# Kernel optimization log

Hardware: AMD Instinct MI355X
Metric: run time of the kernel (lower is better)

## Reference

```python
import jax, jax.numpy as jnp
import numpy as np

B, T, S, E, H, F = 4, 1024, 1024, 512, 8, 2048
D = E // H  # head_dim = 64
SCALE = D ** -0.5
EPS = 1e-5


def setup_inputs() -> dict:
    key = jax.random.key(0)
    ks = jax.random.split(key, 16)
    w = lambda k, shape: jax.random.normal(k, shape, jnp.float32) * 0.02
    inp = {
        'tgt': jax.random.normal(ks[0], (B, T, E), jnp.float32),
        'memory': jax.random.normal(ks[1], (B, S, E), jnp.float32),
    }
    for i, n in enumerate(['sWq', 'sWk', 'sWv', 'sWo', 'cWq', 'cWk', 'cWv', 'cWo']):
        inp[n] = w(ks[2 + i], (E, E))
    for n in ['sbq', 'sbk', 'sbv', 'sbo', 'cbq', 'cbk', 'cbv', 'cbo']:
        inp[n] = jnp.zeros((E,), jnp.float32)
    inp['fW1'] = w(ks[10], (E, F)); inp['fb1'] = jnp.zeros((F,), jnp.float32)
    inp['fW2'] = w(ks[11], (F, E)); inp['fb2'] = jnp.zeros((E,), jnp.float32)
    for n in ['g1', 'g2', 'g3']:
        inp[n] = jnp.ones((E,), jnp.float32)
    for n in ['be1', 'be2', 'be3']:
        inp[n] = jnp.zeros((E,), jnp.float32)
    return inp


def _ln(x, g, b):
    mu = jnp.mean(x, axis=-1, keepdims=True)
    var = jnp.mean(jnp.square(x - mu), axis=-1, keepdims=True)
    return (x - mu) * jax.lax.rsqrt(var + EPS) * g + b


def _mha(xq, xkv, Wq, bq, Wk, bk, Wv, bv, Wo, bo):
    # dense-equivalent of full N^2 edge-list attention (softmax over source nodes per target)
    Bq, Tq, _ = xq.shape
    Skv = xkv.shape[1]
    q = (xq @ Wq + bq).reshape(Bq, Tq, H, D)
    k = (xkv @ Wk + bk).reshape(Bq, Skv, H, D)
    v = (xkv @ Wv + bv).reshape(Bq, Skv, H, D)
    scores = jnp.einsum('bthd,bshd->bhts', q, k) * SCALE
    wts = jax.nn.softmax(scores, axis=-1)
    out = jnp.einsum('bhts,bshd->bthd', wts, v).reshape(Bq, Tq, E)
    return out @ Wo + bo


def reference(tgt, memory,
              sWq, sbq, sWk, sbk, sWv, sbv, sWo, sbo,
              cWq, cbq, cWk, cbk, cWv, cbv, cWo, cbo,
              fW1, fb1, fW2, fb2,
              g1, be1, g2, be2, g3, be3):
    # post-norm decoder layer: self-attn -> cross-attn -> FFN (dropout=0 eval)
    x = _ln(tgt + _mha(tgt, tgt, sWq, sbq, sWk, sbk, sWv, sbv, sWo, sbo), g1, be1)
    x = _ln(x + _mha(x, memory, cWq, cbq, cWk, cbk, cWv, cbv, cWo, cbo), g2, be2)
    ff = jax.nn.relu(x @ fW1 + fb1) @ fW2 + fb2
    x = _ln(x + ff, g3, be3)
    return x
```

## Files before the change

kernel.cpp:

```cpp
#include <hip/hip_runtime.h>

typedef unsigned short ushort_t;
typedef short short8 __attribute__((ext_vector_type(8)));
typedef float float4v __attribute__((ext_vector_type(4)));

__device__ __forceinline__ float bf2f(ushort_t u) {
    union { unsigned int i; float f; } x; x.i = ((unsigned int)u) << 16; return x.f;
}
__device__ __forceinline__ ushort_t f2bf(float f) {
    unsigned int u = __float_as_uint(f);
    unsigned int r = (u + 0x7FFFu + ((u >> 16) & 1u)) >> 16;
    return (ushort_t)r;
}
__device__ __forceinline__ void store_out(float* p, float v) { *p = v; }
__device__ __forceinline__ void store_out(ushort_t* p, float v) { *p = f2bf(v); }

__device__ __forceinline__ void gll16(const ushort_t* g, ushort_t* l) {
    __builtin_amdgcn_global_load_lds(
        (const __attribute__((address_space(1))) void*)g,
        (__attribute__((address_space(3))) void*)l, 16, 0, 0);
}

__global__ void detect_dtype(const ushort_t* __restrict__ tgt, int* __restrict__ flag) {
    __shared__ int red[256];
    const int tid = threadIdx.x;
    int p = 0;
    for (int i = tid; i < 512; i += 256) {
        ushort_t u = tgt[i];
        int e = (u >> 7) & 0xFF;
        if (u == 0 || (e >= 100 && e <= 140)) ++p;
    }
    red[tid] = p; __syncthreads();
    for (int off = 128; off > 0; off >>= 1) {
        if (tid < off) red[tid] += red[tid + off];
        __syncthreads();
    }
    if (tid == 0) flag[0] = (red[0] >= 480) ? 1 : 0;
}

__device__ __forceinline__ bool is_f32(int mode, const int* dflag) {
    return (mode == 2) ? (dflag[0] == 0) : (mode == 0);
}

__global__ __launch_bounds__(256) void prep_all(
    const void* sWq, const void* sWk, const void* sWv, const void* sWo,
    const void* cWq, const void* cWk, const void* cWv, const void* cWo,
    const void* fW1, const void* fW2,
    const void* tgt, const void* mem,
    const void* sbq, const void* sbk, const void* sbv, const void* sbo,
    const void* cbq, const void* cbk, const void* cbv, const void* cbo,
    const void* fb1, const void* fb2,
    ushort_t* __restrict__ wb, ushort_t* __restrict__ tb, ushort_t* __restrict__ mb,
    float* __restrict__ pb, int mode, const int* __restrict__ dflag)
{
    const bool f32 = is_f32(mode, dflag);
    const int tid = threadIdx.x;
    const int id = blockIdx.x;

    if (id < 1024) {
        int z, kt, nt;
        if (id < 512)      { z = id >> 6;  int t = id & 63;  kt = t >> 3; nt = t & 7;  }
        else if (id < 768) { z = 8;        int t = id - 512; kt = t >> 5; nt = t & 31; }
        else               { z = 9;        int t = id - 768; kt = t >> 3; nt = t & 7;  }
        const void* src; ushort_t* dst; int Kd, Nd;
        switch (z) {
            case 0: src = sWq; dst = wb + 0;       Kd = 512;  Nd = 512;  break;
            case 1: src = sWk; dst = wb + 262144;  Kd = 512;  Nd = 512;  break;
            case 2: src = sWv; dst = wb + 524288;  Kd = 512;  Nd = 512;  break;
            case 3: src = sWo; dst = wb + 786432;  Kd = 512;  Nd = 512;  break;
            case 4: src = cWq; dst = wb + 1048576; Kd = 512;  Nd = 512;  break;
            case 5: src = cWk; dst = wb + 1310720; Kd = 512;  Nd = 512;  break;
            case 6: src = cWv; dst = wb + 1572864; Kd = 512;  Nd = 512;  break;
            case 7: src = cWo; dst = wb + 1835008; Kd = 512;  Nd = 512;  break;
            case 8: src = fW1; dst = wb + 2097152; Kd = 512;  Nd = 2048; break;
            default:src = fW2; dst = wb + 3145728; Kd = 2048; Nd = 512;  break;
        }
        const int k0 = kt * 64, n0 = nt * 64;
        __shared__ ushort_t T[64][65];
#pragma unroll
        for (int i = 0; i < 16; ++i) {
            int j = i * 256 + tid;
            int r = j >> 6, c = j & 63;
            float v = f32 ? ((const float*)src)[(size_t)(k0 + r) * Nd + n0 + c]
                          : bf2f(((const ushort_t*)src)[(size_t)(k0 + r) * Nd + n0 + c]);
            T[r][c] = f2bf(v);
        }
        __syncthreads();
#pragma unroll
        for (int i = 0; i < 16; ++i) {
            int j = i * 256 + tid;
            int n = j >> 6, k = j & 63;
            dst[(size_t)(n0 + n) * Kd + k0 + k] = T[k][n];
        }
        return;
    }

    if (id < 3072) {
        const int bid0 = id - 1024;
        const void* src = (bid0 < 1024) ? tgt : mem;
        ushort_t* dst = (bid0 < 1024) ? tb : mb;
        const int bid = bid0 & 1023;
        const int i = (bid * 256 + tid) * 8;
        if (f32) {
            float4 v0 = *(const float4*)((const float*)src + i);
            float4 v1 = *(const float4*)((const float*)src + i + 4);
            ushort_t o[8] = { f2bf(v0.x), f2bf(v0.y), f2bf(v0.z), f2bf(v0.w),
                              f2bf(v1.x), f2bf(v1.y), f2bf(v1.z), f2bf(v1.w) };
            *(uint4*)(dst + i) = *(const uint4*)o;
        } else {
            *(uint4*)(dst + i) = *(const uint4*)((const ushort_t*)src + i);
        }
        return;
    }

    {
        const int i = (id - 3072) * 256 + tid;
        if (i >= 6656) return;
        const void* src; int off;
        if      (i < 512)  { src = sbq; off = i; }
        else if (i < 1024) { src = sbk; off = i - 512; }
        else if (i < 1536) { src = sbv; off = i - 1024; }
        else if (i < 2048) { src = sbo; off = i - 1536; }
        else if (i < 2560) { src = cbq; off = i - 2048; }
        else if (i < 3072) { src = cbk; off = i - 2560; }
        else if (i < 3584) { src = cbv; off = i - 3072; }
        else if (i < 4096) { src = cbo; off = i - 3584; }
        else if (i < 6144) { src = fb1; off = i - 4096; }
        else               { src = fb2; off = i - 6144; }
        pb[i] = f32 ? ((const float*)src)[off] : bf2f(((const ushort_t*)src)[off]);
    }
}

template<typename OutT, bool RELU, int BM, int BN, bool KSPLIT>
__global__ __launch_bounds__(256, (BM == 64) ? 3 : 2) void gemm_tn(
    const ushort_t* __restrict__ A1, const ushort_t* __restrict__ A2,
    int ySplit, int lda,
    const ushort_t* __restrict__ Wt, int ldw,
    const float* __restrict__ bias,
    OutT* __restrict__ C, int ldc, int K,
    OutT* __restrict__ C2)
{
    constexpr int WC = (BM == 64 && BN == 128) ? 4 : 2;
    constexpr int WR = 4 / WC;
    constexpr int MI = BM / (WR * 16);
    constexpr int NI = BN / (WC * 16);
    __shared__ ushort_t As[2][2][BM][32];
    __shared__ ushort_t Bs[2][2][BN][32];
    const int tid = threadIdx.x;
    const int wave = tid >> 6, lane = tid & 63;
    const int quad = lane >> 4, l16 = lane & 15;
    const int m0 = blockIdx.x * BM, n0 = blockIdx.y * BN;
    const int wm = (wave / WC) * (BM / WR);
    const int wn = (wave % WC) * (BN / WC);
    const ushort_t* A = (((int)blockIdx.y) < ySplit) ? A1 : A2;
    const ushort_t* W = Wt;
    OutT* Cw = C;
    bool second = false;
    if (KSPLIT && blockIdx.z) { A += K; W += K; Cw = C2; second = true; }

    float4v acc[MI][NI];
#pragma unroll
    for (int mi = 0; mi < MI; ++mi)
#pragma unroll
        for (int ni = 0; ni < NI; ++ni) {
            acc[mi][ni][0] = 0.f; acc[mi][ni][1] = 0.f;
            acc[mi][ni][2] = 0.f; acc[mi][ni][3] = 0.f;
        }

    const int srow = lane >> 2;
    const int scc  = lane & 3;
    const int sg   = (scc - (lane >> 3)) & 3;
    const ushort_t* aptr0 = A  + (size_t)(m0 + wave * 16 + srow) * lda + sg * 8;
    const ushort_t* aptr1 = A  + (size_t)(m0 + 64 + wave * 16 + srow) * lda + sg * 8;
    const ushort_t* bptr0 = W + (size_t)(n0 + wave * 16 + srow) * ldw + sg * 8;
    const ushort_t* bptr1 = W + (size_t)(n0 + 64 + wave * 16 + srow) * ldw + sg * 8;

    gll16(aptr0,      &As[0][0][wave * 16][0]);
    gll16(aptr0 + 32, &As[0][1][wave * 16][0]);
    if (BM == 128) {
        gll16(aptr1,      &As[0][0][64 + wave * 16][0]);
        gll16(aptr1 + 32, &As[0][1][64 + wave * 16][0]);
    }
    gll16(bptr0,      &Bs[0][0][wave * 16][0]);
    gll16(bptr0 + 32, &Bs[0][1][wave * 16][0]);
    if (BN == 128) {
        gll16(bptr1,      &Bs[0][0][64 + wave * 16][0]);
        gll16(bptr1 + 32, &Bs[0][1][64 + wave * 16][0]);
    }

    const int ca = ((quad + (l16 >> 1)) & 3) * 8;
    int cur = 0;
    for (int k0 = 0; k0 < K; k0 += 64) {
        __syncthreads();
        if (k0 + 64 < K) {
            const int nb = cur ^ 1, ko = k0 + 64;
            gll16(aptr0 + ko,      &As[nb][0][wave * 16][0]);
            gll16(aptr0 + ko + 32, &As[nb][1][wave * 16][0]);
            if (BM == 128) {
                gll16(aptr1 + ko,      &As[nb][0][64 + wave * 16][0]);
                gll16(aptr1 + ko + 32, &As[nb][1][64 + wave * 16][0]);
            }
            gll16(bptr0 + ko,      &Bs[nb][0][wave * 16][0]);
            gll16(bptr0 + ko + 32, &Bs[nb][1][wave * 16][0]);
            if (BN == 128) {
                gll16(bptr1 + ko,      &Bs[nb][0][64 + wave * 16][0]);
                gll16(bptr1 + ko + 32, &Bs[nb][1][64 + wave * 16][0]);
            }
        }
#pragma unroll
        for (int kk = 0; kk < 2; ++kk) {
            short8 af[MI], bfr[NI];
#pragma unroll
            for (int mi = 0; mi < MI; ++mi)
                af[mi] = *(const short8*)(&As[cur][kk][wm + mi * 16 + l16][ca]);
#pragma unroll
            for (int ni = 0; ni < NI; ++ni)
                bfr[ni] = *(const short8*)(&Bs[cur][kk][wn + ni * 16 + l16][ca]);
#pragma unroll
            for (int mi = 0; mi < MI; ++mi)
#pragma unroll
                for (int ni = 0; ni < NI; ++ni)
                    acc[mi][ni] = __builtin_amdgcn_mfma_f32_16x16x32_bf16(
                        af[mi], bfr[ni], acc[mi][ni], 0, 0, 0);
        }
        cur ^= 1;
    }

#pragma unroll
    for (int ni = 0; ni < NI; ++ni) {
        const int col = n0 + wn + ni * 16 + l16;
        const float bv = (KSPLIT && second) ? 0.f : bias[col];
#pragma unroll
        for (int mi = 0; mi < MI; ++mi)
#pragma unroll
            for (int r = 0; r < 4; ++r) {
                const int row = m0 + wm + mi * 16 + quad * 4 + r;
                float v = acc[mi][ni][r] + bv;
                if (RELU) v = fmaxf(v, 0.f);
                store_out(&Cw[(size_t)row * ldc + col], v);
            }
    }
}

__global__ __launch_bounds__(512) void attn_mfma(ushort_t* __restrict__ QKV)
{
    const int S = 1536;
    __shared__ ushort_t PsA[64][72];
    __shared__ ushort_t PsB[64][72];
    __shared__ ushort_t Ks[2][64][72];
    __shared__ ushort_t Vt[2][64][72];

    const int tid  = threadIdx.x;
    const int w    = tid >> 6;
    const int g    = w >> 2;
    const int wq   = w & 3;
    const int lane = tid & 63;
    const int quad = lane >> 4, l16 = lane & 15;
    const int ht   = tid & 255;
    const int qt = blockIdx.x, bh = blockIdx.y;
    const int b = bh >> 3, h = bh & 7;
    const size_t rowQ = (size_t)b * 1024 + qt * 64;
    const size_t kv0  = (size_t)b * 1024;

    const int kr = ht >> 2, kc = (ht & 3) * 16;
    const int sp = ht >> 3, dc = (ht & 7) * 8;
    const int vr0 = sp * 2;
    const int vrg = vr0 >> 3, vrof = vr0 & 7;

    {
        const int r = tid >> 3, c = (tid & 7) * 8;
        *(uint4*)(&PsA[r][c]) = *(const uint4*)(QKV + (rowQ + r) * S + h * 64 + c);
    }
    __syncthreads();
    short8 qf[2];
    qf[0] = *(const short8*)(&PsA[wq * 16 + l16][quad * 8]);
    qf[1] = *(const short8*)(&PsA[wq * 16 + l16][32 + quad * 8]);
    ushort_t (* __restrict__ Ps)[72] = g ? PsB : PsA;

    const float CEXP = 0.125f * 1.44269504f;
    const float MREF = 16.0f * CEXP;
    float lsum[4];
    float4v oacc[4];
#pragma unroll
    for (int r = 0; r < 4; ++r) lsum[r] = 0.f;
#pragma unroll
    for (int n = 0; n < 4; ++n) { oacc[n][0]=0.f; oacc[n][1]=0.f; oacc[n][2]=0.f; oacc[n][3]=0.f; }

    uint4 kA, kB, vA, vB;
    {
        const size_t sr = kv0 + g * 64;
        const ushort_t* ksrc = QKV + (sr + kr) * S + 512 + h * 64 + kc;
        kA = *(const uint4*)(ksrc);
        kB = *(const uint4*)(ksrc + 8);
        const ushort_t* vsrc = QKV + (sr + vr0) * S + 1024 + h * 64 + dc;
        vA = *(const uint4*)(vsrc);
        vB = *(const uint4*)(vsrc + S);
    }

    for (int it = 0; it < 8; ++it) {
        __syncthreads();
        *(uint4*)(&Ks[g][kr][kc])     = kA;
        *(uint4*)(&Ks[g][kr][kc + 8]) = kB;
        {
            const ushort_t* ae = (const ushort_t*)&vA;
            const ushort_t* be = (const ushort_t*)&vB;
#pragma unroll
            for (int j = 0; j < 8; ++j) {
                const int d = dc + j;
                const int cc = (vrg ^ (d >> 4)) & 7;
                *(unsigned int*)(&Vt[g][d][cc * 8 + vrof]) =
                    (unsigned int)ae[j] | ((unsigned int)be[j] << 16);
            }
        }
        __syncthreads();
        if (it < 7) {
            const size_t sr = kv0 + (it + 1) * 128 + g * 64;
            const ushort_t* ksrc = QKV + (sr + kr) * S + 512 + h * 64 + kc;
            kA = *(const uint4*)(ksrc);
            kB = *(const uint4*)(ksrc + 8);
            const ushort_t* vsrc = QKV + (sr + vr0) * S + 1024 + h * 64 + dc;
            vA = *(const uint4*)(vsrc);
            vB = *(const uint4*)(vsrc + S);
        }

        float4v sc[4];
#pragma unroll
        for (int sb = 0; sb < 4; ++sb) {
            float4v z; z[0]=0.f; z[1]=0.f; z[2]=0.f; z[3]=0.f;
            short8 kf0 = *(const short8*)(&Ks[g][sb * 16 + l16][quad * 8]);
            short8 kf1 = *(const short8*)(&Ks[g][sb * 16 + l16][32 + quad * 8]);
            z = __builtin_amdgcn_mfma_f32_16x16x32_bf16(qf[0], kf0, z, 0, 0, 0);
            z = __builtin_amdgcn_mfma_f32_16x16x32_bf16(qf[1], kf1, z, 0, 0, 0);
            sc[sb] = z;
        }

#pragma unroll
        for (int sb = 0; sb < 4; ++sb)
#pragma unroll
            for (int r = 0; r < 4; ++r) {
                float p = exp2f(fmaf(sc[sb][r], CEXP, -MREF));
                lsum[r] += p;
                Ps[wq * 16 + quad * 4 + r][sb * 16 + l16] = f2bf(p);
            }

        short8 pf[2];
        pf[0] = *(const short8*)(&Ps[wq * 16 + l16][quad * 8]);
        pf[1] = *(const short8*)(&Ps[wq * 16 + l16][32 + quad * 8]);
#pragma unroll
        for (int n = 0; n < 4; ++n) {
#pragma unroll
            for (int kc2 = 0; kc2 < 2; ++kc2) {
                const int cc = ((kc2 * 4 + quad) ^ n) & 7;
                short8 vf = *(const short8*)(&Vt[g][n * 16 + l16][cc * 8]);
                oacc[n] = __builtin_amdgcn_mfma_f32_16x16x32_bf16(pf[kc2], vf, oacc[n], 0, 0, 0);
            }
        }
    }

#pragma unroll
    for (int msk = 1; msk < 16; msk <<= 1)
#pragma unroll
        for (int r = 0; r < 4; ++r) lsum[r] += __shfl_xor(lsum[r], msk);

    float* exch = (float*)&Ks[0][0][0];
    float* exl  = (float*)&Vt[0][0][0];
    __syncthreads();
    if (g == 1) {
#pragma unroll
        for (int n = 0; n < 4; ++n)
#pragma unroll
            for (int r = 0; r < 4; ++r)
                exch[((wq * 4 + n) * 4 + r) * 64 + lane] = oacc[n][r];
        if (l16 == 0)
#pragma unroll
            for (int r = 0; r < 4; ++r) exl[wq * 16 + quad * 4 + r] = lsum[r];
    }
    __syncthreads();
    if (g == 0) {
#pragma unroll
        for (int r = 0; r < 4; ++r) lsum[r] += exl[wq * 16 + quad * 4 + r];
        float inv[4];
#pragma unroll
        for (int r = 0; r < 4; ++r) inv[r] = 1.f / lsum[r];
#pragma unroll
        for (int n = 0; n < 4; ++n)
#pragma unroll
            for (int r = 0; r < 4; ++r) {
                float o = oacc[n][r] + exch[((wq * 4 + n) * 4 + r) * 64 + lane];
                const size_t row = rowQ + wq * 16 + quad * 4 + r;
                QKV[row * S + h * 64 + n * 16 + l16] = f2bf(o * inv[r]);
            }
    }
}

template<bool RES_EXT, bool OUT_EXT>
__global__ __launch_bounds__(256) void ln_kernel(
    const void* __restrict__ res,
    const ushort_t* __restrict__ d1, const ushort_t* __restrict__ d2,
    const void* __restrict__ g, const void* __restrict__ be,
    void* __restrict__ out, int mode, const int* __restrict__ dflag)
{
    const int E = 512;
    const bool extf32 = is_f32(mode, dflag);
    const int row = blockIdx.x, tid = threadIdx.x;
    const int wave = tid >> 6, lane = tid & 63;
    const size_t base = (size_t)row * E;
    const int i0 = tid, i1 = tid + 256;

    float r0, r1;
    if (RES_EXT && extf32) {
        r0 = ((const float*)res)[base + i0];
        r1 = ((const float*)res)[base + i1];
    } else {
        r0 = bf2f(((const ushort_t*)res)[base + i0]);
        r1 = bf2f(((const ushort_t*)res)[base + i1]);
    }
    float d0v = bf2f(d1[base + i0]) + bf2f(d2[base + i0]);
    float d1v = bf2f(d1[base + i1]) + bf2f(d2[base + i1]);
    float x0 = r0 + d0v, x1 = r1 + d1v;

    __shared__ float red8[8];
    float s = x0 + x1;
#pragma unroll
    for (int m = 1; m < 64; m <<= 1) s += __shfl_xor(s, m);
    if (lane == 0) red8[wave] = s;
    __syncthreads();
    float mean = (red8[0] + red8[1] + red8[2] + red8[3]) * (1.0f / 512.0f);
    float dd0 = x0 - mean, dd1 = x1 - mean;
    float v = dd0 * dd0 + dd1 * dd1;
#pragma unroll
    for (int m = 1; m < 64; m <<= 1) v += __shfl_xor(v, m);
    if (lane == 0) red8[4 + wave] = v;
    __syncthreads();
    float rstd = rsqrtf((red8[4] + red8[5] + red8[6] + red8[7]) * (1.0f / 512.0f) + 1e-5f);

    float g0, g1v, b0, b1;
    if (extf32) {
        g0 = ((const float*)g)[i0];  g1v = ((const float*)g)[i1];
        b0 = ((const float*)be)[i0]; b1  = ((const float*)be)[i1];
    } else {
        g0 = bf2f(((const ushort_t*)g)[i0]);  g1v = bf2f(((const ushort_t*)g)[i1]);
        b0 = bf2f(((const ushort_t*)be)[i0]); b1  = bf2f(((const ushort_t*)be)[i1]);
    }
    float y0 = dd0 * rstd * g0 + b0;
    float y1 = dd1 * rstd * g1v + b1;
    if (OUT_EXT && extf32) {
        ((float*)out)[base + i0] = y0; ((float*)out)[base + i1] = y1;
    } else {
        ((ushort_t*)out)[base + i0] = f2bf(y0);
        ((ushort_t*)out)[base + i1] = f2bf(y1);
    }
}


extern "C" void kernel_launch(void* const* d_in, const int* in_sizes, int n_in,
                              void* d_out, int out_size, void* d_ws, size_t ws_size,
                              hipStream_t stream) {
    const void* tgt = d_in[0];
    const void* mem = d_in[1];
    const void* sWq = d_in[2];  const void* sWk = d_in[3];
    const void* sWv = d_in[4];  const void* sWo = d_in[5];
    const void* cWq = d_in[6];  const void* cWk = d_in[7];
    const void* cWv = d_in[8];  const void* cWo = d_in[9];
    const void* sbq = d_in[10]; const void* sbk = d_in[11];
    const void* sbv = d_in[12]; const void* sbo = d_in[13];
    const void* cbq = d_in[14]; const void* cbk = d_in[15];
    const void* cbv = d_in[16]; const void* cbo = d_in[17];
    const void* fW1 = d_in[18]; const void* fb1 = d_in[19];
    const void* fW2 = d_in[20]; const void* fb2 = d_in[21];
    const void* g1  = d_in[22]; const void* g2  = d_in[23];
    const void* g3  = d_in[24];
    const void* be1 = d_in[25]; const void* be2 = d_in[26];
    const void* be3 = d_in[27];

    char* ws = (char*)d_ws;
    const size_t MB = 1048576;
    ushort_t* qkv = (ushort_t*)(ws + 0 * MB);
    ushort_t* hb  = (ushort_t*)(ws + 0 * MB);
    ushort_t* pA  = (ushort_t*)(ws + 12 * MB);
    ushort_t* xb  = (ushort_t*)(ws + 16 * MB);
    ushort_t* tb  = (ushort_t*)(ws + 20 * MB);
    ushort_t* mb  = (ushort_t*)(ws + 24 * MB);
    ushort_t* pB  = (ushort_t*)(ws + 20 * MB);
    ushort_t* ofA = (ushort_t*)(ws + 20 * MB);
    ushort_t* ofB = (ushort_t*)(ws + 24 * MB);
    ushort_t* wb  = (ushort_t*)(ws + 28 * MB);
    float*    pb  = (float*)   (ws + 36 * MB);
    int*   dflag  = (int*)     (ws + 36 * MB + 262144);

    const ushort_t* sWqkv_t = wb + 0;
    const ushort_t* sWo_t   = wb + 786432;
    const ushort_t* cWqkv_t = wb + 1048576;
    const ushort_t* cWo_t   = wb + 1835008;
    const ushort_t* fW1_t   = wb + 2097152;
    const ushort_t* fW2_t   = wb + 3145728;

    dim3 blk(256);

    int mode;
    if (in_sizes[0] == 4 * 1024 * 512 * 4)      mode = 0;
    else if (in_sizes[0] == 4 * 1024 * 512 * 2) mode = 1;
    else                                        mode = 2;
    if (mode == 2)
        detect_dtype<<<dim3(1), blk, 0, stream>>>((const ushort_t*)tgt, dflag);

    prep_all<<<dim3(3098), blk, 0, stream>>>(
        sWq, sWk, sWv, sWo, cWq, cWk, cWv, cWo, fW1, fW2,
        tgt, mem, sbq, sbk, sbv, sbo, cbq, cbk, cbv, cbo, fb1, fb2,
        wb, tb, mb, pb, mode, dflag);

    dim3 gattn(16, 32);
    dim3 blk512(512);

    gemm_tn<ushort_t, false, 64, 128, false><<<dim3(64, 12), blk, 0, stream>>>(
        tb, tb, 0, 512, sWqkv_t, 512, pb + 0, qkv, 1536, 512, (ushort_t*)nullptr);
    attn_mfma<<<gattn, blk512, 0, stream>>>(qkv);
    gemm_tn<ushort_t, false, 64, 64, true><<<dim3(64, 8, 2), blk, 0, stream>>>(
        qkv, qkv, 0, 1536, sWo_t, 512, pb + 1536, pA, 512, 256, pB);
    ln_kernel<true, false><<<dim3(4096), blk, 0, stream>>>(
        tgt, pA, pB, g1, be1, xb, mode, dflag);

    gemm_tn<ushort_t, false, 64, 128, false><<<dim3(64, 12), blk, 0, stream>>>(
        xb, mb, 4, 512, cWqkv_t, 512, pb + 2048, qkv, 1536, 512, (ushort_t*)nullptr);
    attn_mfma<<<gattn, blk512, 0, stream>>>(qkv);
    gemm_tn<ushort_t, false, 64, 64, true><<<dim3(64, 8, 2), blk, 0, stream>>>(
        qkv, qkv, 0, 1536, cWo_t, 512, pb + 3584, pA, 512, 256, pB);
    ln_kernel<false, false><<<dim3(4096), blk, 0, stream>>>(
        xb, pA, pB, g2, be2, xb, mode, dflag);

    gemm_tn<ushort_t, true, 128, 128, false><<<dim3(32, 16), blk, 0, stream>>>(
        xb, xb, 0, 512, fW1_t, 512, pb + 4096, hb, 2048, 512, (ushort_t*)nullptr);
    gemm_tn<ushort_t, false, 64, 64, true><<<dim3(64, 8, 2), blk, 0, stream>>>(
        hb, hb, 0, 2048, fW2_t, 2048, pb + 6144, ofA, 512, 1024, ofB);
    ln_kernel<false, true><<<dim3(4096), blk, 0, stream>>>(
        xb, ofA, ofB, g3, be3, d_out, mode, dflag);
}
```

Measured before the change: 266.5 us.

## Shrink FFN GEMM tiles, add BN=32 variant, vectorize LayerNorm loads

Changes the FFN up-projection GEMM from 128x128 to 64x128 tiles and the down-projection from 64x64 to 64x32 tiles, adding a BN=32 path in which only two waves stage B and occupancy is raised to 4. The aim is more blocks to fill the GPU's compute units for these GEMMs. The LayerNorm kernel now gives each thread two adjacent elements, loaded and stored as paired 32-bit or float2 accesses. Smaller tiles cut data reuse and raise global traffic per FLOP, and the BN=32 path depends on the warp layout code handling NI correctly.

```diff
diff --git a/kernel.cpp b/kernel.cpp
--- a/kernel.cpp
+++ b/kernel.cpp
@@ -132,7 +132,8 @@
 }
 
 template<typename OutT, bool RELU, int BM, int BN, bool KSPLIT>
-__global__ __launch_bounds__(256, (BM == 64) ? 3 : 2) void gemm_tn(
+__global__ __launch_bounds__(256, (BM == 64 && BN == 32) ? 4 : ((BM == 64) ? 3 : 2))
+void gemm_tn(
     const ushort_t* __restrict__ A1, const ushort_t* __restrict__ A2,
     int ySplit, int lda,
     const ushort_t* __restrict__ Wt, int ldw,
@@ -158,6 +159,8 @@
     bool second = false;
     if (KSPLIT && blockIdx.z) { A += K; W += K; Cw = C2; second = true; }
 
+    const bool bstage = (BN >= 64) || (wave < 2);
+
     float4v acc[MI][NI];
 #pragma unroll
     for (int mi = 0; mi < MI; ++mi)
@@ -181,8 +184,10 @@
         gll16(aptr1,      &As[0][0][64 + wave * 16][0]);
         gll16(aptr1 + 32, &As[0][1][64 + wave * 16][0]);
     }
-    gll16(bptr0,      &Bs[0][0][wave * 16][0]);
-    gll16(bptr0 + 32, &Bs[0][1][wave * 16][0]);
+    if (bstage) {
+        gll16(bptr0,      &Bs[0][0][wave * 16][0]);
+        gll16(bptr0 + 32, &Bs[0][1][wave * 16][0]);
+    }
     if (BN == 128) {
         gll16(bptr1,      &Bs[0][0][64 + wave * 16][0]);
         gll16(bptr1 + 32, &Bs[0][1][64 + wave * 16][0]);
@@ -200,8 +205,10 @@
                 gll16(aptr1 + ko,      &As[nb][0][64 + wave * 16][0]);
                 gll16(aptr1 + ko + 32, &As[nb][1][64 + wave * 16][0]);
             }
-            gll16(bptr0 + ko,      &Bs[nb][0][wave * 16][0]);
-            gll16(bptr0 + ko + 32, &Bs[nb][1][wave * 16][0]);
+            if (bstage) {
+                gll16(bptr0 + ko,      &Bs[nb][0][wave * 16][0]);
+                gll16(bptr0 + ko + 32, &Bs[nb][1][wave * 16][0]);
+            }
             if (BN == 128) {
                 gll16(bptr1 + ko,      &Bs[nb][0][64 + wave * 16][0]);
                 gll16(bptr1 + ko + 32, &Bs[nb][1][64 + wave * 16][0]);
@@ -405,18 +412,20 @@
     const int row = blockIdx.x, tid = threadIdx.x;
     const int wave = tid >> 6, lane = tid & 63;
     const size_t base = (size_t)row * E;
-    const int i0 = tid, i1 = tid + 256;
+    const int i0 = tid * 2;
 
     float r0, r1;
     if (RES_EXT && extf32) {
-        r0 = ((const float*)res)[base + i0];
-        r1 = ((const float*)res)[base + i1];
+        float2 rv = *(const float2*)((const float*)res + base + i0);
+        r0 = rv.x; r1 = rv.y;
     } else {
-        r0 = bf2f(((const ushort_t*)res)[base + i0]);
-        r1 = bf2f(((const ushort_t*)res)[base + i1]);
-    }
-    float d0v = bf2f(d1[base + i0]) + bf2f(d2[base + i0]);
-    float d1v = bf2f(d1[base + i1]) + bf2f(d2[base + i1]);
+        unsigned int rv = *(const unsigned int*)((const ushort_t*)res + base + i0);
+        r0 = bf2f((ushort_t)rv); r1 = bf2f((ushort_t)(rv >> 16));
+    }
+    unsigned int u1 = *(const unsigned int*)(d1 + base + i0);
+    unsigned int u2 = *(const unsigned int*)(d2 + base + i0);
+    float d0v = bf2f((ushort_t)u1) + bf2f((ushort_t)u2);
+    float d1v = bf2f((ushort_t)(u1 >> 16)) + bf2f((ushort_t)(u2 >> 16));
     float x0 = r0 + d0v, x1 = r1 + d1v;
 
     __shared__ float red8[8];
@@ -436,19 +445,23 @@
 
     float g0, g1v, b0, b1;
     if (extf32) {
-        g0 = ((const float*)g)[i0];  g1v = ((const float*)g)[i1];
-        b0 = ((const float*)be)[i0]; b1  = ((const float*)be)[i1];
+        float2 gv = *(const float2*)((const float*)g + i0);
+        float2 bv = *(const float2*)((const float*)be + i0);
+        g0 = gv.x; g1v = gv.y; b0 = bv.x; b1 = bv.y;
     } else {
-        g0 = bf2f(((const ushort_t*)g)[i0]);  g1v = bf2f(((const ushort_t*)g)[i1]);
-        b0 = bf2f(((const ushort_t*)be)[i0]); b1  = bf2f(((const ushort_t*)be)[i1]);
+        unsigned int gv = *(const unsigned int*)((const ushort_t*)g + i0);
+        unsigned int bv = *(const unsigned int*)((const ushort_t*)be + i0);
+        g0 = bf2f((ushort_t)gv);  g1v = bf2f((ushort_t)(gv >> 16));
+        b0 = bf2f((ushort_t)bv);  b1  = bf2f((ushort_t)(bv >> 16));
     }
     float y0 = dd0 * rstd * g0 + b0;
     float y1 = dd1 * rstd * g1v + b1;
     if (OUT_EXT && extf32) {
-        ((float*)out)[base + i0] = y0; ((float*)out)[base + i1] = y1;
+        float2 ov; ov.x = y0; ov.y = y1;
+        *(float2*)((float*)out + base + i0) = ov;
     } else {
-        ((ushort_t*)out)[base + i0] = f2bf(y0);
-        ((ushort_t*)out)[base + i1] = f2bf(y1);
+        unsigned int ov = (unsigned int)f2bf(y0) | ((unsigned int)f2bf(y1) << 16);
+        *(unsigned int*)((ushort_t*)out + base + i0) = ov;
     }
 }
 
@@ -528,9 +541,9 @@
     ln_kernel<false, false><<<dim3(4096), blk, 0, stream>>>(
         xb, pA, pB, g2, be2, xb, mode, dflag);
 
-    gemm_tn<ushort_t, true, 128, 128, false><<<dim3(32, 16), blk, 0, stream>>>(
+    gemm_tn<ushort_t, true, 64, 128, false><<<dim3(64, 16), blk, 0, stream>>>(
         xb, xb, 0, 512, fW1_t, 512, pb + 4096, hb, 2048, 512, (ushort_t*)nullptr);
-    gemm_tn<ushort_t, false, 64, 64, true><<<dim3(64, 8, 2), blk, 0, stream>>>(
+    gemm_tn<ushort_t, false, 64, 32, true><<<dim3(64, 16, 2), blk, 0, stream>>>(
         hb, hb, 0, 2048, fW2_t, 2048, pb + 6144, ofA, 512, 1024, ofB);
     ln_kernel<false, true><<<dim3(4096), blk, 0, stream>>>(
         xb, ofA, ofB, g3, be3, d_out, mode, dflag);
```

Result: slower. 276.7 us (+3.9%).

## Merge self-attn output projection with cross-attn K/V projection in one launch

Applied to the files above, without the earlier changes.

Adds a combined kernel that runs the self-attention output-projection GEMM blocks and the memory-side K/V projection GEMM blocks of cross-attention together in a single grid, sharing a common LDS pool. The K/V projection depends only on `memory`, so it is hoisted ahead of LayerNorm 1 to fill the GPU alongside the small split-K output projection. The later cross-attention projection launch now computes only the Q columns. This removes one launch and raises occupancy of an under-filled GEMM. The cost is mixed tile shapes in one grid, which can cause load imbalance, and correctness relies on the two halves touching disjoint column ranges of the qkv buffer.

```diff
diff --git a/kernel.cpp b/kernel.cpp
--- a/kernel.cpp
+++ b/kernel.cpp
@@ -128,6 +128,145 @@
         else if (i < 6144) { src = fb1; off = i - 4096; }
         else               { src = fb2; off = i - 6144; }
         pb[i] = f32 ? ((const float*)src)[off] : bf2f(((const ushort_t*)src)[off]);
+    }
+}
+
+template<typename OutT, bool RELU, int BM, int BN, bool KSPLIT>
+__device__ __forceinline__ void gemm_body(ushort_t* pool, int bx, int by, int bz,
+    const ushort_t* __restrict__ A1, const ushort_t* __restrict__ A2,
+    int ySplit, int lda,
+    const ushort_t* __restrict__ Wt, int ldw,
+    const float* __restrict__ bias,
+    OutT* __restrict__ C, int ldc, int K,
+    OutT* __restrict__ C2)
+{
+    constexpr int WC = (BM == 64 && BN == 128) ? 4 : 2;
+    constexpr int WR = 4 / WC;
+    constexpr int MI = BM / (WR * 16);
+    constexpr int NI = BN / (WC * 16);
+    ushort_t* Asp = pool;
+    ushort_t* Bsp = pool + 128 * BM;
+
+    const int tid = threadIdx.x;
+    const int wave = tid >> 6, lane = tid & 63;
+    const int quad = lane >> 4, l16 = lane & 15;
+    const int m0 = bx * BM, n0 = by * BN;
+    const int wm = (wave / WC) * (BM / WR);
+    const int wn = (wave % WC) * (BN / WC);
+    const ushort_t* A = (by < ySplit) ? A1 : A2;
+    const ushort_t* W = Wt;
+    OutT* Cw = C;
+    bool second = false;
+    if (KSPLIT && bz) { A += K; W += K; Cw = C2; second = true; }
+
+    float4v acc[MI][NI];
+#pragma unroll
+    for (int mi = 0; mi < MI; ++mi)
+#pragma unroll
+        for (int ni = 0; ni < NI; ++ni) {
+            acc[mi][ni][0] = 0.f; acc[mi][ni][1] = 0.f;
+            acc[mi][ni][2] = 0.f; acc[mi][ni][3] = 0.f;
+        }
+
+    const int srow = lane >> 2;
+    const int scc  = lane & 3;
+    const int sg   = (scc - (lane >> 3)) & 3;
+    const ushort_t* aptr0 = A + (size_t)(m0 + wave * 16 + srow) * lda + sg * 8;
+    const ushort_t* aptr1 = A + (size_t)(m0 + 64 + wave * 16 + srow) * lda + sg * 8;
+    const ushort_t* bptr0 = W + (size_t)(n0 + wave * 16 + srow) * ldw + sg * 8;
+    const ushort_t* bptr1 = W + (size_t)(n0 + 64 + wave * 16 + srow) * ldw + sg * 8;
+
+    auto As = [&](int buf, int kk, int row) -> ushort_t* {
+        return Asp + (size_t)((buf * 2 + kk) * BM + row) * 32;
+    };
+    auto Bs = [&](int buf, int kk, int row) -> ushort_t* {
+        return Bsp + (size_t)((buf * 2 + kk) * BN + row) * 32;
+    };
+
+    gll16(aptr0,      As(0, 0, wave * 16));
+    gll16(aptr0 + 32, As(0, 1, wave * 16));
+    if (BM == 128) {
+        gll16(aptr1,      As(0, 0, 64 + wave * 16));
+        gll16(aptr1 + 32, As(0, 1, 64 + wave * 16));
+    }
+    gll16(bptr0,      Bs(0, 0, wave * 16));
+    gll16(bptr0 + 32, Bs(0, 1, wave * 16));
+    if (BN == 128) {
+        gll16(bptr1,      Bs(0, 0, 64 + wave * 16));
+        gll16(bptr1 + 32, Bs(0, 1, 64 + wave * 16));
+    }
+
+    const int ca = ((quad + (l16 >> 1)) & 3) * 8;
+    int cur = 0;
+    for (int k0 = 0; k0 < K; k0 += 64) {
+        __syncthreads();
+        if (k0 + 64 < K) {
+            const int nb = cur ^ 1, ko = k0 + 64;
+            gll16(aptr0 + ko,      As(nb, 0, wave * 16));
+            gll16(aptr0 + ko + 32, As(nb, 1, wave * 16));
+            if (BM == 128) {
+                gll16(aptr1 + ko,      As(nb, 0, 64 + wave * 16));
+                gll16(aptr1 + ko + 32, As(nb, 1, 64 + wave * 16));
+            }
+            gll16(bptr0 + ko,      Bs(nb, 0, wave * 16));
+            gll16(bptr0 + ko + 32, Bs(nb, 1, wave * 16));
+            if (BN == 128) {
+                gll16(bptr1 + ko,      Bs(nb, 0, 64 + wave * 16));
+                gll16(bptr1 + ko + 32, Bs(nb, 1, 64 + wave * 16));
+            }
+        }
+#pragma unroll
+        for (int kk = 0; kk < 2; ++kk) {
+            short8 af[MI], bfr[NI];
+#pragma unroll
+            for (int mi = 0; mi < MI; ++mi)
+                af[mi] = *(const short8*)(As(cur, kk, wm + mi * 16 + l16) + ca);
+#pragma unroll
+            for (int ni = 0; ni < NI; ++ni)
+                bfr[ni] = *(const short8*)(Bs(cur, kk, wn + ni * 16 + l16) + ca);
+#pragma unroll
+            for (int mi = 0; mi < MI; ++mi)
+#pragma unroll
+                for (int ni = 0; ni < NI; ++ni)
+                    acc[mi][ni] = __builtin_amdgcn_mfma_f32_16x16x32_bf16(
+                        af[mi], bfr[ni], acc[mi][ni], 0, 0, 0);
+        }
+        cur ^= 1;
+    }
+
+#pragma unroll
+    for (int ni = 0; ni < NI; ++ni) {
+        const int col = n0 + wn + ni * 16 + l16;
+        const float bv = (KSPLIT && second) ? 0.f : bias[col];
+#pragma unroll
+        for (int mi = 0; mi < MI; ++mi)
+#pragma unroll
+            for (int r = 0; r < 4; ++r) {
+                const int row = m0 + wm + mi * 16 + quad * 4 + r;
+                float v = acc[mi][ni][r] + bv;
+                if (RELU) v = fmaxf(v, 0.f);
+                store_out(&Cw[(size_t)row * ldc + col], v);
+            }
+    }
+}
+
+__global__ __launch_bounds__(256, 3) void oproj_ckv(
+    const ushort_t* __restrict__ qkv_in, const ushort_t* __restrict__ sWo_t,
+    const float* __restrict__ bias_o,
+    ushort_t* __restrict__ pA, ushort_t* __restrict__ pB,
+    const ushort_t* __restrict__ mb, const ushort_t* __restrict__ cWqkv_t,
+    const float* __restrict__ bias_c, ushort_t* __restrict__ qkv_out)
+{
+    __shared__ ushort_t pool[24576];
+    const int t = blockIdx.x;
+    if (t < 1024) {
+        gemm_body<ushort_t, false, 64, 64, true>(pool, t & 63, (t >> 6) & 7, t >> 9,
+            qkv_in, qkv_in, 0, 1536, sWo_t, 512, bias_o, pA, 512, 256, pB);
+    } else {
+        const int t2 = t - 1024;
+        gemm_body<ushort_t, false, 64, 128, false>(pool, t2 & 63, 4 + (t2 >> 6), 0,
+            mb, mb, 4, 512, cWqkv_t, 512, bias_c, qkv_out, 1536, 512,
+            (ushort_t*)nullptr);
     }
 }
 
@@ -515,12 +654,12 @@
     gemm_tn<ushort_t, false, 64, 128, false><<<dim3(64, 12), blk, 0, stream>>>(
         tb, tb, 0, 512, sWqkv_t, 512, pb + 0, qkv, 1536, 512, (ushort_t*)nullptr);
     attn_mfma<<<gattn, blk512, 0, stream>>>(qkv);
-    gemm_tn<ushort_t, false, 64, 64, true><<<dim3(64, 8, 2), blk, 0, stream>>>(
-        qkv, qkv, 0, 1536, sWo_t, 512, pb + 1536, pA, 512, 256, pB);
+    oproj_ckv<<<dim3(1536), blk, 0, stream>>>(
+        qkv, sWo_t, pb + 1536, pA, pB, mb, cWqkv_t, pb + 2048, qkv);
     ln_kernel<true, false><<<dim3(4096), blk, 0, stream>>>(
         tgt, pA, pB, g1, be1, xb, mode, dflag);
 
-    gemm_tn<ushort_t, false, 64, 128, false><<<dim3(64, 12), blk, 0, stream>>>(
+    gemm_tn<ushort_t, false, 64, 128, false><<<dim3(64, 4), blk, 0, stream>>>(
         xb, mb, 4, 512, cWqkv_t, 512, pb + 2048, qkv, 1536, 512, (ushort_t*)nullptr);
     attn_mfma<<<gattn, blk512, 0, stream>>>(qkv);
     gemm_tn<ushort_t, false, 64, 64, true><<<dim3(64, 8, 2), blk, 0, stream>>>(
```

After: 272.1 us. 2.1% more time.
